# Optimization experiments

Hardware: AMD Instinct MI355X
Metric: run time of the kernel (lower is better)

## Reference

```python
import jax, jax.numpy as jnp
import numpy as np


def _idft_matrix(n):
    # IDFT_n[j,k] = (1/n) * exp(+2*pi*i*j*k/n)  (matches 1/N * DFT**(-1) in source)
    jk = np.outer(np.arange(n), np.arange(n))
    return jnp.asarray((np.exp(2j * np.pi * jk / n) / n).astype(np.complex64))


def setup_inputs() -> dict:
    key = jax.random.key(0)
    B, Y, X = 64, 512, 512
    inp = jax.random.normal(key, (B, Y, X, 2), dtype=jnp.float32)
    return {"inp": inp}


def reference(inp) -> jnp.ndarray:
    B, Y, X, _ = inp.shape
    # pack real/imag channels into complex64
    c = jax.lax.complex(inp[..., 0], inp[..., 1])  # [B, Y, X]
    IDFT_y = _idft_matrix(Y)  # [Y, Y]
    IDFT_x = _idft_matrix(X)  # [X, X]
    # IDFT along Y axis: 'db,abc->adc'
    res1 = jnp.einsum('db,abc->adc', IDFT_y, c)
    # IDFT along X axis then magnitude: 'cd,abc->abd'
    out = jnp.abs(jnp.einsum('cd,abc->abd', IDFT_x, res1))
    return out[..., None]  # [B, Y, X, 1]
```

## Files before the change

### kernel.cpp

```cpp
#include <hip/hip_runtime.h>
#include <hip/hip_fp16.h>
#include <math.h>


#define TWO_PI_F 6.283185307179586f

__device__ __forceinline__ float2 cmul(float2 a, float2 b) {
    return make_float2(a.x * b.x - a.y * b.y, a.x * b.y + a.y * b.x);
}
__device__ __forceinline__ float2 cadd(float2 a, float2 b) { return make_float2(a.x + b.x, a.y + b.y); }
__device__ __forceinline__ float2 csub(float2 a, float2 b) { return make_float2(a.x - b.x, a.y - b.y); }
__device__ __forceinline__ float2 csq(float2 a) { return make_float2(a.x * a.x - a.y * a.y, 2.f * a.x * a.y); }
__device__ __forceinline__ unsigned rev6(unsigned v) { return __brev(v) >> 26; }

__device__ __forceinline__ void fft512(float2* r, float2 A, int l) {
    const float S = 0.70710678118654752f;
    {
        float2 t0 = A;
        float2 t1 = cmul(A, make_float2(S, S));
        float2 t2 = make_float2(-A.y, A.x);
        float2 t3 = cmul(A, make_float2(-S, S));
        float2 u, v;
        u = r[0]; v = r[4]; r[0] = cadd(u, v); r[4] = cmul(csub(u, v), t0);
        u = r[1]; v = r[5]; r[1] = cadd(u, v); r[5] = cmul(csub(u, v), t1);
        u = r[2]; v = r[6]; r[2] = cadd(u, v); r[6] = cmul(csub(u, v), t2);
        u = r[3]; v = r[7]; r[3] = cadd(u, v); r[7] = cmul(csub(u, v), t3);
    }
    float2 A2 = csq(A);
    {
        float2 A2i = make_float2(-A2.y, A2.x);
        float2 u, v;
        u = r[0]; v = r[2]; r[0] = cadd(u, v); r[2] = cmul(csub(u, v), A2);
        u = r[1]; v = r[3]; r[1] = cadd(u, v); r[3] = cmul(csub(u, v), A2i);
        u = r[4]; v = r[6]; r[4] = cadd(u, v); r[6] = cmul(csub(u, v), A2);
        u = r[5]; v = r[7]; r[5] = cadd(u, v); r[7] = cmul(csub(u, v), A2i);
    }
    float2 A4 = csq(A2);
    {
        float2 u, v;
        u = r[0]; v = r[1]; r[0] = cadd(u, v); r[1] = cmul(csub(u, v), A4);
        u = r[2]; v = r[3]; r[2] = cadd(u, v); r[3] = cmul(csub(u, v), A4);
        u = r[4]; v = r[5]; r[4] = cadd(u, v); r[5] = cmul(csub(u, v), A4);
        u = r[6]; v = r[7]; r[6] = cadd(u, v); r[7] = cmul(csub(u, v), A4);
    }
    float2 P = csq(A4);
    #pragma unroll
    for (int mi = 0; mi < 6; ++mi) {
        const int m = 32 >> mi;
        const bool hi = (l & m) != 0;
        #pragma unroll
        for (int k = 0; k < 8; ++k) {
            float2 o;
            o.x = __shfl_xor(r[k].x, m);
            o.y = __shfl_xor(r[k].y, m);
            float2 sum = cadd(r[k], o);
            float2 dif = cmul(csub(r[k], o), P);
            r[k].x = hi ? dif.x : sum.x;
            r[k].y = hi ? dif.y : sum.y;
        }
        if (mi < 5) P = csq(P);
    }
}

__global__ __launch_bounds__(512)
void fft_y_kernel(const float2* __restrict__ in, __half* __restrict__ wsh) {
    __shared__ float2 tile[8 * 512];
    const int t = threadIdx.x;
    const int w = t >> 6, l = t & 63;
    const int g = t & 3, q = t >> 2;
    const int x0 = blockIdx.x * 8;
    const int b  = blockIdx.y;

    const float2* src = in + ((size_t)b << 18) + x0;
    #pragma unroll
    for (int it = 0; it < 4; ++it) {
        const int y = it * 128 + q;
        const float4 v = *(const float4*)(src + ((size_t)y << 9) + 2 * g);
        const int ys = y ^ (4 * g);
        tile[(2 * g) * 512 + ys]     = make_float2(v.x, v.y);
        tile[(2 * g + 1) * 512 + ys] = make_float2(v.z, v.w);
    }
    __syncthreads();

    float sA, cA;
    sincosf(TWO_PI_F * (float)l * (1.0f / 512.0f), &sA, &cA);
    float2 r[8];
    const int sw = 4 * (w >> 1);
    #pragma unroll
    for (int k = 0; k < 8; ++k)
        r[k] = tile[w * 512 + ((k * 64 + l) ^ sw)];

    fft512(r, make_float2(cA, sA), l);

    const float s = 1.0f / 512.0f;
    __half* dst = wsh + (((size_t)(b * 512 + x0 + w)) << 10) + rev6((unsigned)l) * 16;
    union { uint4 u; __half2 h[4]; } a0, a1;
    a0.h[0] = __floats2half2_rn(r[0].x * s, r[0].y * s);
    a0.h[1] = __floats2half2_rn(r[4].x * s, r[4].y * s);
    a0.h[2] = __floats2half2_rn(r[2].x * s, r[2].y * s);
    a0.h[3] = __floats2half2_rn(r[6].x * s, r[6].y * s);
    a1.h[0] = __floats2half2_rn(r[1].x * s, r[1].y * s);
    a1.h[1] = __floats2half2_rn(r[5].x * s, r[5].y * s);
    a1.h[2] = __floats2half2_rn(r[3].x * s, r[3].y * s);
    a1.h[3] = __floats2half2_rn(r[7].x * s, r[7].y * s);
    *(uint4*)dst       = a0.u;
    *(uint4*)(dst + 8) = a1.u;
}

__global__ __launch_bounds__(512)
void fft_x_mag_kernel(const __half* __restrict__ wsh, float* __restrict__ out) {
    __shared__ uint tile[8 * 512];
    const int t = threadIdx.x;
    const int w = t >> 6, l = t & 63;
    const int f0 = blockIdx.x * 8;
    const int b  = blockIdx.y;

    {
        const __half* src = wsh + ((size_t)b << 19) + ((size_t)t << 10) + f0 * 2;
        const uint4 ua = *(const uint4*)(src);
        const uint4 ub = *(const uint4*)(src + 8);
        tile[0 * 512 + t] = ua.x;
        tile[1 * 512 + t] = ua.y;
        tile[2 * 512 + t] = ua.z;
        tile[3 * 512 + t] = ua.w;
        tile[4 * 512 + t] = ub.x;
        tile[5 * 512 + t] = ub.y;
        tile[6 * 512 + t] = ub.z;
        tile[7 * 512 + t] = ub.w;
    }
    __syncthreads();

    float sA, cA;
    sincosf(TWO_PI_F * (float)l * (1.0f / 512.0f), &sA, &cA);
    float2 r[8];
    #pragma unroll
    for (int k = 0; k < 8; ++k) {
        uint p = tile[w * 512 + k * 64 + l];
        r[k] = __half22float2(*(const __half2*)&p);
    }

    fft512(r, make_float2(cA, sA), l);

    const float s = 1.0f / 512.0f;
    float m0 = sqrtf(r[0].x * r[0].x + r[0].y * r[0].y) * s;
    float m1 = sqrtf(r[4].x * r[4].x + r[4].y * r[4].y) * s;
    float m2 = sqrtf(r[2].x * r[2].x + r[2].y * r[2].y) * s;
    float m3 = sqrtf(r[6].x * r[6].x + r[6].y * r[6].y) * s;
    float m4 = sqrtf(r[1].x * r[1].x + r[1].y * r[1].y) * s;
    float m5 = sqrtf(r[5].x * r[5].x + r[5].y * r[5].y) * s;
    float m6 = sqrtf(r[3].x * r[3].x + r[3].y * r[3].y) * s;
    float m7 = sqrtf(r[7].x * r[7].x + r[7].y * r[7].y) * s;

    float* orow = out + (((size_t)(b * 512 + f0 + w)) << 9) + rev6((unsigned)l) * 8;
    *(float4*)(orow + 0) = make_float4(m0, m1, m2, m3);
    *(float4*)(orow + 4) = make_float4(m4, m5, m6, m7);
}

extern "C" void kernel_launch(void* const* d_in, const int* in_sizes, int n_in,
                              void* d_out, int out_size, void* d_ws, size_t ws_size,
                              hipStream_t stream) {
    const float2* in = (const float2*)d_in[0];
    __half* wsh = (__half*)d_ws;
    float* out = (float*)d_out;

    fft_y_kernel<<<dim3(64, 64), 512, 0, stream>>>(in, wsh);
    fft_x_mag_kernel<<<dim3(64, 64), 512, 0, stream>>>(wsh, out);
}
```

Before: 276.5 us.

## Process four batches per block with register prefetch of next tile

Each block now loops over four batch slices instead of one, and the grid shrinks by four in y. Global loads for the next slice go into registers before the FFT on the current slice, so memory latency overlaps with compute. Twiddle setup is hoisted out of the loop. It adds two barriers per iteration, raises register pressure, and leaves fewer blocks (1024 per kernel) to fill the GPU, with a launch-bounds occupancy hint of 8.

```diff
diff --git a/kernel.cpp b/kernel.cpp
--- a/kernel.cpp
+++ b/kernel.cpp
@@ -62,63 +62,100 @@
     }
 }
 
-__global__ __launch_bounds__(512)
+__global__ __launch_bounds__(512, 8)
 void fft_y_kernel(const float2* __restrict__ in, __half* __restrict__ wsh) {
     __shared__ float2 tile[8 * 512];
     const int t = threadIdx.x;
     const int w = t >> 6, l = t & 63;
     const int g = t & 3, q = t >> 2;
     const int x0 = blockIdx.x * 8;
-    const int b  = blockIdx.y;
-
-    const float2* src = in + ((size_t)b << 18) + x0;
-    #pragma unroll
-    for (int it = 0; it < 4; ++it) {
-        const int y = it * 128 + q;
-        const float4 v = *(const float4*)(src + ((size_t)y << 9) + 2 * g);
-        const int ys = y ^ (4 * g);
-        tile[(2 * g) * 512 + ys]     = make_float2(v.x, v.y);
-        tile[(2 * g + 1) * 512 + ys] = make_float2(v.z, v.w);
-    }
-    __syncthreads();
+    const int b0 = blockIdx.y * 4;
 
     float sA, cA;
     sincosf(TWO_PI_F * (float)l * (1.0f / 512.0f), &sA, &cA);
-    float2 r[8];
+    const float2 Atw = make_float2(cA, sA);
     const int sw = 4 * (w >> 1);
-    #pragma unroll
-    for (int k = 0; k < 8; ++k)
-        r[k] = tile[w * 512 + ((k * 64 + l) ^ sw)];
-
-    fft512(r, make_float2(cA, sA), l);
-
     const float s = 1.0f / 512.0f;
-    __half* dst = wsh + (((size_t)(b * 512 + x0 + w)) << 10) + rev6((unsigned)l) * 16;
-    union { uint4 u; __half2 h[4]; } a0, a1;
-    a0.h[0] = __floats2half2_rn(r[0].x * s, r[0].y * s);
-    a0.h[1] = __floats2half2_rn(r[4].x * s, r[4].y * s);
-    a0.h[2] = __floats2half2_rn(r[2].x * s, r[2].y * s);
-    a0.h[3] = __floats2half2_rn(r[6].x * s, r[6].y * s);
-    a1.h[0] = __floats2half2_rn(r[1].x * s, r[1].y * s);
-    a1.h[1] = __floats2half2_rn(r[5].x * s, r[5].y * s);
-    a1.h[2] = __floats2half2_rn(r[3].x * s, r[3].y * s);
-    a1.h[3] = __floats2half2_rn(r[7].x * s, r[7].y * s);
-    *(uint4*)dst       = a0.u;
-    *(uint4*)(dst + 8) = a1.u;
-}
-
-__global__ __launch_bounds__(512)
+
+    float4 v0, v1, v2, v3;
+    {
+        const float2* src = in + ((size_t)b0 << 18) + x0;
+        v0 = *(const float4*)(src + ((size_t)(0 * 128 + q) << 9) + 2 * g);
+        v1 = *(const float4*)(src + ((size_t)(1 * 128 + q) << 9) + 2 * g);
+        v2 = *(const float4*)(src + ((size_t)(2 * 128 + q) << 9) + 2 * g);
+        v3 = *(const float4*)(src + ((size_t)(3 * 128 + q) << 9) + 2 * g);
+    }
+
+    for (int tt = 0; tt < 4; ++tt) {
+        {
+            int ys;
+            ys = (0 * 128 + q) ^ (4 * g);
+            tile[(2 * g) * 512 + ys]     = make_float2(v0.x, v0.y);
+            tile[(2 * g + 1) * 512 + ys] = make_float2(v0.z, v0.w);
+            ys = (1 * 128 + q) ^ (4 * g);
+            tile[(2 * g) * 512 + ys]     = make_float2(v1.x, v1.y);
+            tile[(2 * g + 1) * 512 + ys] = make_float2(v1.z, v1.w);
+            ys = (2 * 128 + q) ^ (4 * g);
+            tile[(2 * g) * 512 + ys]     = make_float2(v2.x, v2.y);
+            tile[(2 * g + 1) * 512 + ys] = make_float2(v2.z, v2.w);
+            ys = (3 * 128 + q) ^ (4 * g);
+            tile[(2 * g) * 512 + ys]     = make_float2(v3.x, v3.y);
+            tile[(2 * g + 1) * 512 + ys] = make_float2(v3.z, v3.w);
+        }
+        if (tt < 3) {
+            const float2* src = in + ((size_t)(b0 + tt + 1) << 18) + x0;
+            v0 = *(const float4*)(src + ((size_t)(0 * 128 + q) << 9) + 2 * g);
+            v1 = *(const float4*)(src + ((size_t)(1 * 128 + q) << 9) + 2 * g);
+            v2 = *(const float4*)(src + ((size_t)(2 * 128 + q) << 9) + 2 * g);
+            v3 = *(const float4*)(src + ((size_t)(3 * 128 + q) << 9) + 2 * g);
+        }
+        __syncthreads();
+
+        float2 r[8];
+        #pragma unroll
+        for (int k = 0; k < 8; ++k)
+            r[k] = tile[w * 512 + ((k * 64 + l) ^ sw)];
+
+        fft512(r, Atw, l);
+
+        __half* dst = wsh + (((size_t)((b0 + tt) * 512 + x0 + w)) << 10) + rev6((unsigned)l) * 16;
+        union { uint4 u; __half2 h[4]; } a0, a1;
+        a0.h[0] = __floats2half2_rn(r[0].x * s, r[0].y * s);
+        a0.h[1] = __floats2half2_rn(r[4].x * s, r[4].y * s);
+        a0.h[2] = __floats2half2_rn(r[2].x * s, r[2].y * s);
+        a0.h[3] = __floats2half2_rn(r[6].x * s, r[6].y * s);
+        a1.h[0] = __floats2half2_rn(r[1].x * s, r[1].y * s);
+        a1.h[1] = __floats2half2_rn(r[5].x * s, r[5].y * s);
+        a1.h[2] = __floats2half2_rn(r[3].x * s, r[3].y * s);
+        a1.h[3] = __floats2half2_rn(r[7].x * s, r[7].y * s);
+        *(uint4*)dst       = a0.u;
+        *(uint4*)(dst + 8) = a1.u;
+
+        __syncthreads();
+    }
+}
+
+__global__ __launch_bounds__(512, 8)
 void fft_x_mag_kernel(const __half* __restrict__ wsh, float* __restrict__ out) {
     __shared__ uint tile[8 * 512];
     const int t = threadIdx.x;
     const int w = t >> 6, l = t & 63;
     const int f0 = blockIdx.x * 8;
-    const int b  = blockIdx.y;
-
-    {
-        const __half* src = wsh + ((size_t)b << 19) + ((size_t)t << 10) + f0 * 2;
-        const uint4 ua = *(const uint4*)(src);
-        const uint4 ub = *(const uint4*)(src + 8);
+    const int b0 = blockIdx.y * 4;
+
+    float sA, cA;
+    sincosf(TWO_PI_F * (float)l * (1.0f / 512.0f), &sA, &cA);
+    const float2 Atw = make_float2(cA, sA);
+    const float s = 1.0f / 512.0f;
+
+    uint4 ua, ub;
+    {
+        const __half* src = wsh + ((size_t)b0 << 19) + ((size_t)t << 10) + f0 * 2;
+        ua = *(const uint4*)(src);
+        ub = *(const uint4*)(src + 8);
+    }
+
+    for (int tt = 0; tt < 4; ++tt) {
         tile[0 * 512 + t] = ua.x;
         tile[1 * 512 + t] = ua.y;
         tile[2 * 512 + t] = ua.z;
@@ -127,33 +164,37 @@
         tile[5 * 512 + t] = ub.y;
         tile[6 * 512 + t] = ub.z;
         tile[7 * 512 + t] = ub.w;
-    }
-    __syncthreads();
-
-    float sA, cA;
-    sincosf(TWO_PI_F * (float)l * (1.0f / 512.0f), &sA, &cA);
-    float2 r[8];
-    #pragma unroll
-    for (int k = 0; k < 8; ++k) {
-        uint p = tile[w * 512 + k * 64 + l];
-        r[k] = __half22float2(*(const __half2*)&p);
-    }
-
-    fft512(r, make_float2(cA, sA), l);
-
-    const float s = 1.0f / 512.0f;
-    float m0 = sqrtf(r[0].x * r[0].x + r[0].y * r[0].y) * s;
-    float m1 = sqrtf(r[4].x * r[4].x + r[4].y * r[4].y) * s;
-    float m2 = sqrtf(r[2].x * r[2].x + r[2].y * r[2].y) * s;
-    float m3 = sqrtf(r[6].x * r[6].x + r[6].y * r[6].y) * s;
-    float m4 = sqrtf(r[1].x * r[1].x + r[1].y * r[1].y) * s;
-    float m5 = sqrtf(r[5].x * r[5].x + r[5].y * r[5].y) * s;
-    float m6 = sqrtf(r[3].x * r[3].x + r[3].y * r[3].y) * s;
-    float m7 = sqrtf(r[7].x * r[7].x + r[7].y * r[7].y) * s;
-
-    float* orow = out + (((size_t)(b * 512 + f0 + w)) << 9) + rev6((unsigned)l) * 8;
-    *(float4*)(orow + 0) = make_float4(m0, m1, m2, m3);
-    *(float4*)(orow + 4) = make_float4(m4, m5, m6, m7);
+        if (tt < 3) {
+            const __half* src = wsh + ((size_t)(b0 + tt + 1) << 19) + ((size_t)t << 10) + f0 * 2;
+            ua = *(const uint4*)(src);
+            ub = *(const uint4*)(src + 8);
+        }
+        __syncthreads();
+
+        float2 r[8];
+        #pragma unroll
+        for (int k = 0; k < 8; ++k) {
+            uint p = tile[w * 512 + k * 64 + l];
+            r[k] = __half22float2(*(const __half2*)&p);
+        }
+
+        fft512(r, Atw, l);
+
+        float m0 = sqrtf(r[0].x * r[0].x + r[0].y * r[0].y) * s;
+        float m1 = sqrtf(r[4].x * r[4].x + r[4].y * r[4].y) * s;
+        float m2 = sqrtf(r[2].x * r[2].x + r[2].y * r[2].y) * s;
+        float m3 = sqrtf(r[6].x * r[6].x + r[6].y * r[6].y) * s;
+        float m4 = sqrtf(r[1].x * r[1].x + r[1].y * r[1].y) * s;
+        float m5 = sqrtf(r[5].x * r[5].x + r[5].y * r[5].y) * s;
+        float m6 = sqrtf(r[3].x * r[3].x + r[3].y * r[3].y) * s;
+        float m7 = sqrtf(r[7].x * r[7].x + r[7].y * r[7].y) * s;
+
+        float* orow = out + (((size_t)((b0 + tt) * 512 + f0 + w)) << 9) + rev6((unsigned)l) * 8;
+        *(float4*)(orow + 0) = make_float4(m0, m1, m2, m3);
+        *(float4*)(orow + 4) = make_float4(m4, m5, m6, m7);
+
+        __syncthreads();
+    }
 }
 
 extern "C" void kernel_launch(void* const* d_in, const int* in_sizes, int n_in,
@@ -163,6 +204,6 @@
     __half* wsh = (__half*)d_ws;
     float* out = (float*)d_out;
 
-    fft_y_kernel<<<dim3(64, 64), 512, 0, stream>>>(in, wsh);
-    fft_x_mag_kernel<<<dim3(64, 64), 512, 0, stream>>>(wsh, out);
-}
+    fft_y_kernel<<<dim3(64, 16), 512, 0, stream>>>(in, wsh);
+    fft_x_mag_kernel<<<dim3(64, 16), 512, 0, stream>>>(wsh, out);
+}
```

Result: slower. 532.8 us (+92.7%).
